# Optimization experiments

Hardware: AMD Instinct MI355X
Metric: run time of the kernel (lower is better)

Reference implementation:

```python
import jax, jax.numpy as jnp
import numpy as np

B, N, D, H = 4, 2048, 256, 4
DH = D // H          # 64
SCALE = DH ** (-0.5)
LN_EPS = 1e-5


def setup_inputs() -> dict:
    key = jax.random.key(0)
    ks = jax.random.split(key, 16)
    g = lambda k, shape, fan_in: jax.random.normal(k, shape, jnp.float32) / np.sqrt(fan_in)
    # Weights stored as [in, out] (pre-transposed vs torch Linear)
    return {
        "x0": jax.random.normal(ks[0], (B, N, D), jnp.float32),
        "x1": jax.random.normal(ks[1], (B, N, D), jnp.float32),
        "Wqk": g(ks[2], (D, D), D), "bqk": jnp.zeros((D,), jnp.float32),
        "Wv": g(ks[3], (D, D), D), "bv": jnp.zeros((D,), jnp.float32),
        "Wout": g(ks[4], (D, D), D), "bout": jnp.zeros((D,), jnp.float32),
        "Wf1": g(ks[5], (2 * D, 2 * D), 2 * D), "bf1": jnp.zeros((2 * D,), jnp.float32),
        "ln_g": jnp.ones((2 * D,), jnp.float32), "ln_b": jnp.zeros((2 * D,), jnp.float32),
        "Wf2": g(ks[6], (2 * D, D), 2 * D), "bf2": jnp.zeros((D,), jnp.float32),
    }


def _split_heads(t):
    # [B,N,D] -> [B,H,N,DH]
    b, n, _ = t.shape
    return t.reshape(b, n, H, DH).transpose(0, 2, 1, 3)


def _merge_heads(t):
    # [B,H,N,DH] -> [B,N,D]
    b, h, n, dh = t.shape
    return t.transpose(0, 2, 1, 3).reshape(b, n, h * dh)


def _layernorm(x, g, b):
    mu = jnp.mean(x, axis=-1, keepdims=True)
    var = jnp.mean(jnp.square(x - mu), axis=-1, keepdims=True)
    return (x - mu) * jax.lax.rsqrt(var + LN_EPS) * g + b


def reference(x0, x1, Wqk, bqk, Wv, bv, Wout, bout, Wf1, bf1, ln_g, ln_b, Wf2, bf2):
    qk0 = _split_heads(x0 @ Wqk + bqk)   # [B,H,N,DH]
    qk1 = _split_heads(x1 @ Wqk + bqk)
    v0 = _split_heads(x0 @ Wv + bv)
    v1 = _split_heads(x1 @ Wv + bv)

    ss = SCALE ** 0.5
    sim = jnp.einsum('bhid,bhjd->bhij', qk0 * ss, qk1 * ss)  # shared score matrix
    attn01 = jax.nn.softmax(sim, axis=-1)   # normalize over j
    attn10 = jax.nn.softmax(sim, axis=-2)   # normalize over i (== softmax(sim^T) transposed)
    m0 = jnp.einsum('bhij,bhjd->bhid', attn01, v1)
    m1 = jnp.einsum('bhji,bhjd->bhid', attn10, v0)

    m0 = _merge_heads(m0) @ Wout + bout   # [B,N,D]
    m1 = _merge_heads(m1) @ Wout + bout

    def ffn(x):
        h = x @ Wf1 + bf1                 # [B,N,2D]
        h = jax.nn.gelu(_layernorm(h, ln_g, ln_b), approximate=False)
        return h @ Wf2 + bf2              # [B,N,D]

    y0 = x0 + ffn(jnp.concatenate([x0, m0], axis=-1))
    y1 = x1 + ffn(jnp.concatenate([x1, m1], axis=-1))
    return (y0, y1)
```

## Files before the change

kernel.cpp:

```cpp
#include <hip/hip_runtime.h>
#include <hip/hip_bf16.h>
#include <math.h>

typedef __bf16 bf16;
typedef __attribute__((ext_vector_type(8))) __bf16 bf16x8;
typedef __attribute__((ext_vector_type(4))) __bf16 bf16x4;
typedef __attribute__((ext_vector_type(2))) __bf16 bf16x2;
typedef __attribute__((ext_vector_type(4))) float f32x4;
typedef __attribute__((ext_vector_type(16))) float f32x16;
typedef __attribute__((ext_vector_type(4))) unsigned u32x4;

#define MFMA(a,b,c)   __builtin_amdgcn_mfma_f32_16x16x32_bf16(a,b,c,0,0,0)
#define MFMA32(a,b,c) __builtin_amdgcn_mfma_f32_32x32x16_bf16(a,b,c,0,0,0)

static constexpr int Bb = 4, Nn = 2048, Hh = 4;
static constexpr float SS2 = 0.4246609001440095f;

__device__ __forceinline__ void lds16(const bf16* src, bf16* dst) {
  __builtin_amdgcn_global_load_lds(
      (const __attribute__((address_space(1))) void*)src,
      (__attribute__((address_space(3))) void*)dst, 16, 0, 0);
}

__device__ __forceinline__ f32x16 zero16() {
  f32x16 t;
#pragma unroll
  for (int i = 0; i < 16; ++i) t[i] = 0.f;
  return t;
}

__global__ __launch_bounds__(256) void prep_k(
    const float* Wqk, const float* Wv, const float* Wout, const float* bout,
    const float* Wf1, const float* Wf2, const float* x0, const float* x1,
    bf16* wqkv_t, bf16* wout_b, bf16* wfold_t, bf16* wf1b_t, bf16* wf2_t,
    bf16* xb0, bf16* xb1) {
  int id = blockIdx.x * 256 + threadIdx.x;
  if (id < 65536) { int k = id >> 8, n = id & 255; wqkv_t[n*256 + k] = (bf16)Wqk[id]; return; }
  id -= 65536;
  if (id < 65536) { int k = id >> 8, n = id & 255; wqkv_t[(256 + n)*256 + k] = (bf16)Wv[id]; return; }
  id -= 65536;
  if (id < 98304) {
    if (id < 65536) { wout_b[id] = (bf16)Wout[id]; }
    else { int id3 = id - 65536; int r = id3 >> 8, k = id3 & 255;
           wout_b[(256 + r)*256 + k] = (r == 0) ? (bf16)bout[k] : (bf16)0.f; }
    return; }
  id -= 98304;
  if (id < 131072) { int o = id & 511, k = id >> 9; wfold_t[o*512 + k] = (bf16)Wf1[k*512 + o]; return; }
  id -= 131072;
  if (id < 131072) { int o = id & 511, k = id >> 9; wf1b_t[o*256 + k] = (bf16)Wf1[(256 + k)*512 + o]; return; }
  id -= 131072;
  if (id < 131072) { int k = id >> 8, n = id & 255; wf2_t[n*512 + k] = (bf16)Wf2[id]; return; }
  id -= 131072;
  if (id < 1048576) {
    const float* xs = (id < 524288) ? x0 : x1;
    bf16* xd = (id < 524288) ? xb0 : xb1;
    int j = (id < 524288) ? id : id - 524288;
    f32x4 v = *reinterpret_cast<const f32x4*>(&xs[(size_t)j * 4]);
    bf16x4 o; o[0] = (bf16)v[0]; o[1] = (bf16)v[1]; o[2] = (bf16)v[2]; o[3] = (bf16)v[3];
    *reinterpret_cast<bf16x4*>(&xd[(size_t)j * 4]) = o;
  }
}

__global__ __launch_bounds__(256, 2) void qkvfold_k(
    const bf16* xb0, const bf16* xb1, const bf16* wqkv_t,
    const float* bqk, const float* bv,
    bf16* qks0, bf16* qks1, bf16* vT0, bf16* vT1,
    const bf16* wout_b, const bf16* wf1b_t, const float* bf1,
    bf16* wfold_t, float* bfold) {
  const int fid = blockIdx.x;
  const bool fold = fid >= 512;
  int bx, by, bz;
  if (!fold) {
    bx = ((fid & 7) << 3) + ((fid >> 3) & 7);
    by = (fid >> 6) & 3;
    bz = fid >> 8;
  } else {
    int id = fid - 512;
    bx = id % 3; by = id / 3; bz = 0;
  }

  const bf16* Aa = fold ? wout_b : (bz ? xb1 : xb0);
  const bf16* Wt = fold ? wf1b_t : wqkv_t;

  const int tid = threadIdx.x;
  const int lane = tid & 63;
  const int w = tid >> 6;
  const int wr = w >> 1, wc = w & 1;
  const int m0r = bx * 128;
  const int n0 = by * 128;
  const int r15 = lane & 15, g = lane >> 4, rb = r15 & 7;
  const int l3 = lane >> 3, l7 = lane & 7;
  const int swzc = (l7 ^ l3) * 8;

  __shared__ bf16 At[2][8192];
  __shared__ bf16 Bt[2][8192];

  const bf16* aA = Aa + (size_t)(m0r + w*32 + l3) * 256 + swzc;
  const bf16* bB = Wt + (size_t)(n0 + w*32 + l3) * 256 + swzc;
  const int adst = (w*32) * 64;

  auto stage = [&](int buf, int kc) {
#pragma unroll
    for (int i = 0; i < 4; i++)
      lds16(aA + kc*64 + (size_t)i * 8 * 256, &At[buf][adst + i*512]);
#pragma unroll
    for (int i = 0; i < 4; i++)
      lds16(bB + kc*64 + (size_t)i * 8 * 256, &Bt[buf][adst + i*512]);
  };

  f32x4 acc[4][4];
#pragma unroll
  for (int i = 0; i < 4; i++)
#pragma unroll
    for (int j = 0; j < 4; j++) acc[i][j] = f32x4{0.f, 0.f, 0.f, 0.f};

  const int rx0 = ((0*4 + g) ^ rb) << 4;
  const int rx1 = ((1*4 + g) ^ rb) << 4;

  auto compute = [&](int cur) {
    const char* Ap = (const char*)&At[cur][0];
    const char* Bp = (const char*)&Bt[cur][0];
    __builtin_amdgcn_s_setprio(1);
#pragma unroll
    for (int ks = 0; ks < 2; ++ks) {
      const int rx = ks ? rx1 : rx0;
      bf16x8 af[4], bfr[4];
#pragma unroll
      for (int mf = 0; mf < 4; ++mf)
        af[mf] = *reinterpret_cast<const bf16x8*>(Ap + (wr*64 + mf*16 + r15) * 128 + rx);
#pragma unroll
      for (int nf = 0; nf < 4; ++nf)
        bfr[nf] = *reinterpret_cast<const bf16x8*>(Bp + (wc*64 + nf*16 + r15) * 128 + rx);
#pragma unroll
      for (int mf = 0; mf < 4; ++mf)
#pragma unroll
        for (int nf = 0; nf < 4; ++nf)
          acc[mf][nf] = MFMA(af[mf], bfr[nf], acc[mf][nf]);
    }
    __builtin_amdgcn_s_setprio(0);
  };

  stage(0, 0);
  int cur = 0;
  for (int kc = 0; kc < 3; ++kc) {
    stage(cur ^ 1, kc + 1);
    asm volatile("s_waitcnt vmcnt(8)" ::: "memory");
    __builtin_amdgcn_sched_barrier(0);
    __builtin_amdgcn_s_barrier();
    __builtin_amdgcn_sched_barrier(0);
    compute(cur);
    asm volatile("s_waitcnt lgkmcnt(0)" ::: "memory");
    __builtin_amdgcn_sched_barrier(0);
    __builtin_amdgcn_s_barrier();
    __builtin_amdgcn_sched_barrier(0);
    cur ^= 1;
  }
  asm volatile("s_waitcnt vmcnt(0)" ::: "memory");
  __builtin_amdgcn_sched_barrier(0);
  __builtin_amdgcn_s_barrier();
  __builtin_amdgcn_sched_barrier(0);
  compute(cur);

  if (!fold) {
    bf16* qks = bz ? qks1 : qks0;
    bf16* vT  = bz ? vT1  : vT0;
#pragma unroll
    for (int mf = 0; mf < 4; ++mf)
#pragma unroll
      for (int nf = 0; nf < 4; ++nf) {
        f32x4 c = acc[mf][nf];
        int cg = n0 + wc*64 + nf*16 + r15;
#pragma unroll
        for (int r = 0; r < 4; ++r) {
          int rg = m0r + wr*64 + mf*16 + g*4 + r;
          int b = rg >> 11, n = rg & 2047;
          if (cg < 256) {
            float val = (c[r] + bqk[cg]) * SS2;
            int h = cg >> 6, dh = cg & 63;
            qks[(((size_t)(b*Hh + h)) * Nn + n) * 64 + dh] = (bf16)val;
          } else {
            int c2 = cg - 256;
            float val = c[r] + bv[c2];
            int h = c2 >> 6, dh = c2 & 63;
            vT[(((size_t)(b*Hh + h)) * 64 + dh) * Nn + n] = (bf16)val;
          }
        }
      }
  } else {
#pragma unroll
    for (int mf = 0; mf < 4; ++mf)
#pragma unroll
      for (int nf = 0; nf < 4; ++nf) {
        f32x4 c = acc[mf][nf];
        int cg = n0 + wc*64 + nf*16 + r15;
#pragma unroll
        for (int r = 0; r < 4; ++r) {
          int rg = m0r + wr*64 + mf*16 + g*4 + r;
          if (rg < 256) wfold_t[(size_t)cg * 512 + 256 + rg] = (bf16)c[r];
          else if (rg == 256) bfold[cg] = c[r] + bf1[cg];
        }
      }
  }
}

template<int MODE, int BN, int MINW, int REMAP>
__global__ __launch_bounds__(256, MINW) void gemm_k(
    const bf16* Aa0, const bf16* Aa1, const bf16* Ac0, const bf16* Ac1,
    const bf16* Wt, const float* bias,
    bf16* ob0, bf16* ob1, float* of0, float* of1) {
  constexpr int KD  = 512;
  constexpr int LDA = (MODE == 4) ? 512 : 256;
  constexpr int NKC = KD / 64;
  constexpr int NF  = BN / 32;

  int bx = blockIdx.x, by = blockIdx.y, bz = blockIdx.z;
  if constexpr (REMAP == 1) {
    int id = blockIdx.x + 64 * (blockIdx.y + 4 * blockIdx.z);
    bx = ((id & 7) << 3) + ((id >> 3) & 7);
    by = (id >> 6) & 3;
    bz = id >> 8;
  }

  const bf16* Aa = bz ? Aa1 : Aa0;
  const bf16* Ac = bz ? Ac1 : Ac0;
  bf16*  ob = bz ? ob1 : ob0;
  float* of = bz ? of1 : of0;

  const int tid = threadIdx.x;
  const int lane = tid & 63;
  const int w = tid >> 6;
  const int wr = w >> 1, wc = w & 1;
  const int m0r = bx * 128;
  const int n0 = by * BN;
  const int r15 = lane & 15, g = lane >> 4, rb = r15 & 7;
  const int l3 = lane >> 3, l7 = lane & 7;
  const int swzc = (l7 ^ l3) * 8;

  __shared__ bf16 At[2][8192];
  __shared__ bf16 Bt[2][BN * 64];

  const bf16* aA = Aa + (size_t)(m0r + w*32 + l3) * LDA + swzc;
  const bf16* aC = (MODE == 3) ? (Ac + (size_t)(m0r + w*32 + l3) * 256 + swzc) : nullptr;
  const bf16* bB = Wt + (size_t)(n0 + w*(BN/4) + l3) * KD + swzc;
  const int adst = (w*32) * 64;
  const int bdst = (w*(BN/4)) * 64;

  auto stage = [&](int buf, int kc) {
    const bf16* ab; int kcol;
    if constexpr (MODE == 3) {
      if (kc < 4) { ab = aA; kcol = kc * 64; } else { ab = aC; kcol = (kc - 4) * 64; }
    } else { ab = aA; kcol = kc * 64; }
#pragma unroll
    for (int i = 0; i < 4; i++)
      lds16(ab + kcol + (size_t)i * 8 * LDA, &At[buf][adst + i*512]);
#pragma unroll
    for (int i = 0; i < NF; i++)
      lds16(bB + kc*64 + (size_t)i * 8 * KD, &Bt[buf][bdst + i*512]);
  };

  f32x4 acc[4][NF];
#pragma unroll
  for (int i = 0; i < 4; i++)
#pragma unroll
    for (int j = 0; j < NF; j++) acc[i][j] = f32x4{0.f, 0.f, 0.f, 0.f};

  const int rx0 = ((0*4 + g) ^ rb) << 4;
  const int rx1 = ((1*4 + g) ^ rb) << 4;

  auto compute = [&](int cur) {
    const char* Ap = (const char*)&At[cur][0];
    const char* Bp = (const char*)&Bt[cur][0];
    __builtin_amdgcn_s_setprio(1);
#pragma unroll
    for (int ks = 0; ks < 2; ++ks) {
      const int rx = ks ? rx1 : rx0;
      bf16x8 af[4], bfr[NF];
#pragma unroll
      for (int mf = 0; mf < 4; ++mf)
        af[mf] = *reinterpret_cast<const bf16x8*>(Ap + (wr*64 + mf*16 + r15) * 128 + rx);
#pragma unroll
      for (int nf = 0; nf < NF; ++nf)
        bfr[nf] = *reinterpret_cast<const bf16x8*>(Bp + (wc*(BN/2) + nf*16 + r15) * 128 + rx);
#pragma unroll
      for (int mf = 0; mf < 4; ++mf)
#pragma unroll
        for (int nf = 0; nf < NF; ++nf)
          acc[mf][nf] = MFMA(af[mf], bfr[nf], acc[mf][nf]);
    }
    __builtin_amdgcn_s_setprio(0);
  };

  stage(0, 0);
  int cur = 0;
  for (int kc = 0; kc < NKC - 1; ++kc) {
    stage(cur ^ 1, kc + 1);
    if constexpr (NF == 4) asm volatile("s_waitcnt vmcnt(8)" ::: "memory");
    else                   asm volatile("s_waitcnt vmcnt(6)" ::: "memory");
    __builtin_amdgcn_sched_barrier(0);
    __builtin_amdgcn_s_barrier();
    __builtin_amdgcn_sched_barrier(0);
    compute(cur);
    asm volatile("s_waitcnt lgkmcnt(0)" ::: "memory");
    __builtin_amdgcn_sched_barrier(0);
    __builtin_amdgcn_s_barrier();
    __builtin_amdgcn_sched_barrier(0);
    cur ^= 1;
  }
  asm volatile("s_waitcnt vmcnt(0)" ::: "memory");
  __builtin_amdgcn_sched_barrier(0);
  __builtin_amdgcn_s_barrier();
  __builtin_amdgcn_sched_barrier(0);
  compute(cur);

#pragma unroll
  for (int mf = 0; mf < 4; ++mf)
#pragma unroll
    for (int nf = 0; nf < NF; ++nf) {
      f32x4 c = acc[mf][nf];
      int cg = n0 + wc*(BN/2) + nf*16 + r15;
#pragma unroll
      for (int r = 0; r < 4; ++r) {
        int rg = m0r + wr*64 + mf*16 + g*4 + r;
        if constexpr (MODE == 3) {
          ob[(size_t)rg * 512 + cg] = (bf16)(c[r] + bias[cg]);
        } else {
          of[(size_t)rg * 256 + cg] = c[r] + bias[cg] + (float)Ac[(size_t)rg * 256 + cg];
        }
      }
    }
}

__global__ __launch_bounds__(512, 4) void attn_k(
    const bf16* qks0, const bf16* qks1, const bf16* vT0, const bf16* vT1,
    bf16* m0o, bf16* m1o) {
  const int B = blockIdx.x + 16 * (blockIdx.y + 16 * blockIdx.z);
  const int xcd = B & 7, kk = B >> 3;
  const int group = 4 * xcd + (kk >> 4);
  const int it = kk & 15;
  const int bh = group & 15, dir = group >> 4;

  const bf16* Q  = (dir ? qks1 : qks0) + (size_t)bh * (Nn * 64);
  const bf16* Kp = (dir ? qks0 : qks1) + (size_t)bh * (Nn * 64);
  const bf16* Vp = (dir ? vT0  : vT1 ) + (size_t)bh * (64 * Nn);
  bf16* out = dir ? m1o : m0o;
  const int b = bh >> 2, h = bh & 3;

  const int tid = threadIdx.x, lane = tid & 63, w = tid >> 6;
  const int ig = w >> 1, hj = w & 1;
  const int l31 = lane & 31, hi = lane >> 5, xr = l31 & 7;
  const int iw = it * 128 + ig * 32;

  __shared__ char smem[65536];
  bf16* KV = (bf16*)smem;
  const int kbase = hj * 8192;
  const int vbase = 16384 + hj * 8192;

  bf16x8 qf[4];
#pragma unroll
  for (int kt = 0; kt < 4; ++kt)
    qf[kt] = *reinterpret_cast<const bf16x8*>(
        &Q[(size_t)(iw + l31) * 64 + kt*16 + hi*8]);

  f32x16 acc[2]; acc[0] = zero16(); acc[1] = zero16();
  float rsum = 0.f;

  const int l3 = lane >> 3, l7 = lane & 7;
  const int swz = ((l7 ^ l3) * 8);
  const bf16* ks0 = Kp + (size_t)(ig*16 +     l3) * 64 + swz;
  const bf16* ks1 = Kp + (size_t)(ig*16 + 8 + l3) * 64 + swz;
  const bf16* vs0 = Vp + (size_t)(ig*16 +     l3) * 2048 + swz;
  const bf16* vs1 = Vp + (size_t)(ig*16 + 8 + l3) * 2048 + swz;
  const int kd0 = (ig*16    ) * 64;
  const int kd1 = (ig*16 + 8) * 64;

  auto stage = [&](int buf, int j0) {
    lds16(ks0 + (size_t)j0 * 64, KV + kbase + buf*4096 + kd0);
    lds16(ks1 + (size_t)j0 * 64, KV + kbase + buf*4096 + kd1);
    lds16(vs0 + j0,              KV + vbase + buf*4096 + kd0);
    lds16(vs1 + j0,              KV + vbase + buf*4096 + kd1);
  };

  int kby[2][4], vby[2][4];
#pragma unroll
  for (int jm = 0; jm < 2; ++jm)
#pragma unroll
    for (int kt = 0; kt < 4; ++kt)
      kby[jm][kt] = (jm*32 + l31) * 128 + (((2*kt + hi) ^ xr) << 4);
#pragma unroll
  for (int nt = 0; nt < 2; ++nt)
#pragma unroll
    for (int gg = 0; gg < 4; ++gg)
      vby[nt][gg] = (nt*32 + l31) * 128 + (((2*gg + hi) ^ xr) << 4);

  auto compute_tile = [&](int cur) {
    const char* Kb = (const char*)(KV + kbase + cur*4096);
    const char* Vb = (const char*)(KV + vbase + cur*4096);
    f32x16 st[2];
    __builtin_amdgcn_s_setprio(1);
#pragma unroll
    for (int jm = 0; jm < 2; ++jm) {
      f32x16 t = zero16();
#pragma unroll
      for (int kt = 0; kt < 4; ++kt) {
        bf16x8 kf = *reinterpret_cast<const bf16x8*>(Kb + kby[jm][kt]);
        t = MFMA32(kf, qf[kt], t);
      }
      st[jm] = t;
    }
    __builtin_amdgcn_s_setprio(0);
    bf16x8 pa[4];
#pragma unroll
    for (int jm = 0; jm < 2; ++jm) {
      unsigned dw[8];
#pragma unroll
      for (int s = 0; s < 8; ++s) {
        float e0 = __builtin_amdgcn_exp2f(st[jm][2*s]);
        float e1 = __builtin_amdgcn_exp2f(st[jm][2*s + 1]);
        rsum += e0 + e1;
        asm("v_cvt_pk_bf16_f32 %0, %1, %2" : "=v"(dw[s]) : "v"(e0), "v"(e1));
      }
#pragma unroll
      for (int kt2 = 0; kt2 < 2; ++kt2) {
        unsigned a0 = dw[4*kt2 + 0], b0 = dw[4*kt2 + 2];
        unsigned a1 = dw[4*kt2 + 1], b1 = dw[4*kt2 + 3];
        asm volatile("v_permlane32_swap_b32 %0, %1" : "+v"(a0), "+v"(b0));
        asm volatile("v_permlane32_swap_b32 %0, %1" : "+v"(a1), "+v"(b1));
        u32x4 uu; uu[0] = a0; uu[1] = a1; uu[2] = b0; uu[3] = b1;
        pa[jm*2 + kt2] = __builtin_bit_cast(bf16x8, uu);
      }
    }
    __builtin_amdgcn_s_setprio(1);
#pragma unroll
    for (int gg = 0; gg < 4; ++gg) {
#pragma unroll
      for (int nt = 0; nt < 2; ++nt) {
        bf16x8 vf = *reinterpret_cast<const bf16x8*>(Vb + vby[nt][gg]);
        acc[nt] = MFMA32(pa[gg], vf, acc[nt]);
      }
    }
    __builtin_amdgcn_s_setprio(0);
  };

  const int jt0 = hj << 4;
  stage(0, jt0 << 6);
  int cur = 0;
  for (int t = 0; t < 15; ++t) {
    stage(cur ^ 1, (jt0 + t + 1) << 6);
    asm volatile("s_waitcnt vmcnt(4)" ::: "memory");
    __builtin_amdgcn_sched_barrier(0);
    __builtin_amdgcn_s_barrier();
    __builtin_amdgcn_sched_barrier(0);
    compute_tile(cur);
    asm volatile("s_waitcnt lgkmcnt(0)" ::: "memory");
    __builtin_amdgcn_sched_barrier(0);
    __builtin_amdgcn_s_barrier();
    __builtin_amdgcn_sched_barrier(0);
    cur ^= 1;
  }
  asm volatile("s_waitcnt vmcnt(0)" ::: "memory");
  __builtin_amdgcn_sched_barrier(0);
  __builtin_amdgcn_s_barrier();
  __builtin_amdgcn_sched_barrier(0);
  compute_tile(cur);

  rsum += __shfl_xor(rsum, 32);
  __syncthreads();
  float* Ex = (float*)smem;
  if (hj == 1) {
#pragma unroll
    for (int nt = 0; nt < 2; ++nt)
#pragma unroll
      for (int r = 0; r < 16; ++r)
        Ex[(ig*33 + nt*16 + r) * 64 + lane] = acc[nt][r];
    Ex[(ig*33 + 32) * 64 + lane] = rsum;
  }
  __syncthreads();
  if (hj == 0) {
    float tot = rsum + Ex[(ig*33 + 32) * 64 + lane];
    float* Rt2 = (float*)(smem + 49152);
    if (lane < 32) Rt2[ig*32 + l31] = tot;
    f32x4 rv[4];
#pragma unroll
    for (int q = 0; q < 4; ++q)
      rv[q] = *reinterpret_cast<const f32x4*>(&Rt2[ig*32 + 8*q + 4*hi]);
#pragma unroll
    for (int r = 0; r < 16; ++r) {
      float inv = 1.0f / rv[r >> 2][r & 3];
      int row = iw + (r & 3) + 8*(r >> 2) + 4*hi;
#pragma unroll
      for (int nt = 0; nt < 2; ++nt) {
        float o = acc[nt][r] + Ex[(ig*33 + nt*16 + r) * 64 + lane];
        int col = h*64 + nt*32 + l31;
        out[((size_t)b * Nn + row) * 256 + col] = (bf16)(o * inv);
      }
    }
  }
}

__global__ __launch_bounds__(256) void ln_gelu_k(
    bf16* hg, const float* g, const float* bb) {
  const int row = (blockIdx.x << 2) + (threadIdx.x >> 6);
  const int lane = threadIdx.x & 63;
  bf16* hr = hg + (size_t)row * 512 + lane * 8;
  bf16x8 v = *reinterpret_cast<const bf16x8*>(hr);
  float f[8];
  float s = 0.f, sq = 0.f;
#pragma unroll
  for (int i = 0; i < 8; ++i) { f[i] = (float)v[i]; s += f[i]; sq += f[i]*f[i]; }
#pragma unroll
  for (int m = 1; m < 64; m <<= 1) { s += __shfl_xor(s, m); sq += __shfl_xor(sq, m); }
  float mu = s * (1.f / 512.f);
  float var = sq * (1.f / 512.f) - mu * mu;
  float rsv = rsqrtf(var + 1e-5f);
  f32x4 g0 = *reinterpret_cast<const f32x4*>(&g[lane*8]);
  f32x4 g1 = *reinterpret_cast<const f32x4*>(&g[lane*8 + 4]);
  f32x4 b0 = *reinterpret_cast<const f32x4*>(&bb[lane*8]);
  f32x4 b1 = *reinterpret_cast<const f32x4*>(&bb[lane*8 + 4]);
  bf16x8 o;
#pragma unroll
  for (int i = 0; i < 8; ++i) {
    float gv = (i < 4) ? g0[i] : g1[i-4];
    float bv = (i < 4) ? b0[i] : b1[i-4];
    float xn = (f[i] - mu) * rsv * gv + bv;
    float ge = 0.5f * xn * (1.f + erff(xn * 0.70710678118f));
    o[i] = (bf16)ge;
  }
  *reinterpret_cast<bf16x8*>(hr) = o;
}

extern "C" void kernel_launch(void* const* d_in, const int* in_sizes, int n_in,
                              void* d_out, int out_size, void* d_ws, size_t ws_size,
                              hipStream_t stream) {
  (void)in_sizes; (void)n_in; (void)out_size; (void)ws_size;
  const float* x0   = (const float*)d_in[0];
  const float* x1   = (const float*)d_in[1];
  const float* Wqk  = (const float*)d_in[2];
  const float* bqk  = (const float*)d_in[3];
  const float* Wv   = (const float*)d_in[4];
  const float* bv   = (const float*)d_in[5];
  const float* Wout = (const float*)d_in[6];
  const float* bout = (const float*)d_in[7];
  const float* Wf1  = (const float*)d_in[8];
  const float* bf1  = (const float*)d_in[9];
  const float* ln_g = (const float*)d_in[10];
  const float* ln_b = (const float*)d_in[11];
  const float* Wf2  = (const float*)d_in[12];
  const float* bf2  = (const float*)d_in[13];
  float* y = (float*)d_out;

  bf16* p = (bf16*)d_ws;
  bf16* wqkv_t = p; p += 131072;
  bf16* wout_b = p; p += 98304;
  bf16* wfold_t = p; p += 262144;
  bf16* wf1b_t = p; p += 131072;
  bf16* wf2_t  = p; p += 131072;
  float* bfold = (float*)p; p += 1024;
  bf16* xb0  = p; p += 2097152;
  bf16* xb1  = p; p += 2097152;
  bf16* qks0 = p; p += 2097152;
  bf16* qks1 = p; p += 2097152;
  bf16* vT0  = p; p += 2097152;
  bf16* vT1  = p; p += 2097152;
  bf16* m0   = p; p += 2097152;
  bf16* m1   = p; p += 2097152;
  bf16* hg0  = p; p += 4194304;
  bf16* hg1  = p; p += 4194304;

  dim3 blk(256);
  prep_k<<<6528, blk, 0, stream>>>(Wqk, Wv, Wout, bout, Wf1, Wf2, x0, x1,
                                   wqkv_t, wout_b, wfold_t, wf1b_t, wf2_t, xb0, xb1);
  qkvfold_k<<<dim3(524), blk, 0, stream>>>(
      xb0, xb1, wqkv_t, bqk, bv, qks0, qks1, vT0, vT1,
      wout_b, wf1b_t, bf1, wfold_t, bfold);
  attn_k<<<dim3(16, 16, 2), dim3(512), 0, stream>>>(qks0, qks1, vT0, vT1, m0, m1);
  gemm_k<3,128,2,1><<<dim3(64, 4, 2), blk, 0, stream>>>(
      xb0, xb1, m0, m1, wfold_t, bfold,
      hg0, hg1, nullptr, nullptr);
  ln_gelu_k<<<dim3(4096), blk, 0, stream>>>(hg0, ln_g, ln_b);
  gemm_k<4,64,3,0><<<dim3(64, 4, 2), blk, 0, stream>>>(
      hg0, hg1, xb0, xb1, wf2_t, bf2,
      nullptr, nullptr, y, y + 2097152);
}
```

Before: 120.6 us.

## Fuse LayerNorm and GELU into the first FFN GEMM epilogue

Adds a dedicated GEMM kernel in which each 512-thread block computes a 64-row tile across all 512 output columns. This lets the block reduce per-row mean and variance in-register and through LDS, then apply LayerNorm, affine and exact GELU before writing bf16. It removes the separate ln_gelu pass and the extra read and write of the hidden activations, and drops the MODE 3 branch from the generic GEMM. The second FFN GEMM also switches to the remapped block ordering. The cost is a large LDS footprint, about 144KB double-buffered, which allows only one block per CU. It also brings a cross-wave reduction with extra barriers in the epilogue and a full weight re-read per block.

Result: slower. 124.2 us (+3.0%).

```diff
diff --git a/kernel.cpp b/kernel.cpp
--- a/kernel.cpp
+++ b/kernel.cpp
@@ -203,6 +203,174 @@
   }
 }
 
+__global__ __launch_bounds__(512, 2) void gemm3f_k(
+    const bf16* Aa0, const bf16* Aa1, const bf16* Ac0, const bf16* Ac1,
+    const bf16* Wt, const float* bias,
+    const float* lng, const float* lnb,
+    bf16* ob0, bf16* ob1) {
+  const int id = blockIdx.x;
+  const int bz = id >> 7, bx = id & 127;
+  const bf16* Aa = bz ? Aa1 : Aa0;
+  const bf16* Ac = bz ? Ac1 : Ac0;
+  bf16* ob = bz ? ob1 : ob0;
+
+  const int tid = threadIdx.x;
+  const int lane = tid & 63;
+  const int w = tid >> 6;
+  const int m0r = bx * 64;
+  const int r15 = lane & 15, g = lane >> 4, rb = r15 & 7;
+  const int l3 = lane >> 3, l7 = lane & 7;
+  const int swzc = (l7 ^ l3) * 8;
+
+  __shared__ bf16 At[2][4096];
+  __shared__ bf16 Bt[2][32768];
+
+  const bf16* aA = Aa + (size_t)(m0r + w*8 + l3) * 256 + swzc;
+  const bf16* aC = Ac + (size_t)(m0r + w*8 + l3) * 256 + swzc;
+  const bf16* bB = Wt + (size_t)(w*64 + l3) * 512 + swzc;
+  const int adst = (w*8) * 64;
+  const int bdst = (w*64) * 64;
+
+  auto stage = [&](int buf, int kc) {
+    const bf16* ab = (kc < 4) ? aA : aC;
+    const int kcol = (kc < 4) ? kc*64 : (kc - 4)*64;
+    lds16(ab + kcol, &At[buf][adst]);
+#pragma unroll
+    for (int i = 0; i < 8; i++)
+      lds16(bB + kc*64 + (size_t)i * 8 * 512, &Bt[buf][bdst + i*512]);
+  };
+
+  f32x4 acc[4][4];
+#pragma unroll
+  for (int i = 0; i < 4; i++)
+#pragma unroll
+    for (int j = 0; j < 4; j++) acc[i][j] = f32x4{0.f, 0.f, 0.f, 0.f};
+
+  const int rx0 = ((0*4 + g) ^ rb) << 4;
+  const int rx1 = ((1*4 + g) ^ rb) << 4;
+
+  auto compute = [&](int cur) {
+    const char* Ap = (const char*)&At[cur][0];
+    const char* Bp = (const char*)&Bt[cur][0];
+    __builtin_amdgcn_s_setprio(1);
+#pragma unroll
+    for (int ks = 0; ks < 2; ++ks) {
+      const int rx = ks ? rx1 : rx0;
+      bf16x8 af[4], bfr[4];
+#pragma unroll
+      for (int mf = 0; mf < 4; ++mf)
+        af[mf] = *reinterpret_cast<const bf16x8*>(Ap + (mf*16 + r15) * 128 + rx);
+#pragma unroll
+      for (int nf = 0; nf < 4; ++nf)
+        bfr[nf] = *reinterpret_cast<const bf16x8*>(Bp + (w*64 + nf*16 + r15) * 128 + rx);
+#pragma unroll
+      for (int mf = 0; mf < 4; ++mf)
+#pragma unroll
+        for (int nf = 0; nf < 4; ++nf)
+          acc[mf][nf] = MFMA(af[mf], bfr[nf], acc[mf][nf]);
+    }
+    __builtin_amdgcn_s_setprio(0);
+  };
+
+  stage(0, 0);
+  int cur = 0;
+  for (int kc = 0; kc < 7; ++kc) {
+    stage(cur ^ 1, kc + 1);
+    asm volatile("s_waitcnt vmcnt(9)" ::: "memory");
+    __builtin_amdgcn_sched_barrier(0);
+    __builtin_amdgcn_s_barrier();
+    __builtin_amdgcn_sched_barrier(0);
+    compute(cur);
+    asm volatile("s_waitcnt lgkmcnt(0)" ::: "memory");
+    __builtin_amdgcn_sched_barrier(0);
+    __builtin_amdgcn_s_barrier();
+    __builtin_amdgcn_sched_barrier(0);
+    cur ^= 1;
+  }
+  asm volatile("s_waitcnt vmcnt(0)" ::: "memory");
+  __builtin_amdgcn_sched_barrier(0);
+  __builtin_amdgcn_s_barrier();
+  __builtin_amdgcn_sched_barrier(0);
+  compute(cur);
+
+  float bch[4];
+#pragma unroll
+  for (int nf = 0; nf < 4; ++nf) bch[nf] = bias[w*64 + nf*16 + r15];
+
+  float s_[4][4], s2_[4][4];
+#pragma unroll
+  for (int mf = 0; mf < 4; ++mf)
+#pragma unroll
+    for (int r = 0; r < 4; ++r) {
+      float s = 0.f, s2 = 0.f;
+#pragma unroll
+      for (int nf = 0; nf < 4; ++nf) {
+        float v = acc[mf][nf][r] + bch[nf];
+        s += v; s2 += v * v;
+      }
+      s_[mf][r] = s; s2_[mf][r] = s2;
+    }
+#pragma unroll
+  for (int mf = 0; mf < 4; ++mf)
+#pragma unroll
+    for (int r = 0; r < 4; ++r) {
+#pragma unroll
+      for (int m = 1; m < 16; m <<= 1) {
+        s_[mf][r]  += __shfl_xor(s_[mf][r],  m);
+        s2_[mf][r] += __shfl_xor(s2_[mf][r], m);
+      }
+    }
+  __syncthreads();
+  float* sred  = (float*)&At[0][0];
+  float* rstat = sred + 1024;
+  if (r15 == 0) {
+#pragma unroll
+    for (int mf = 0; mf < 4; ++mf)
+#pragma unroll
+      for (int r = 0; r < 4; ++r) {
+        int row = mf*16 + g*4 + r;
+        sred[(w*64 + row)*2    ] = s_[mf][r];
+        sred[(w*64 + row)*2 + 1] = s2_[mf][r];
+      }
+  }
+  __syncthreads();
+  if (tid < 64) {
+    float S = 0.f, S2 = 0.f;
+#pragma unroll
+    for (int wv = 0; wv < 8; ++wv) {
+      S  += sred[(wv*64 + tid)*2];
+      S2 += sred[(wv*64 + tid)*2 + 1];
+    }
+    float mu = S * (1.f/512.f);
+    float var = S2 * (1.f/512.f) - mu*mu;
+    rstat[tid*2]     = mu;
+    rstat[tid*2 + 1] = rsqrtf(var + 1e-5f);
+  }
+  __syncthreads();
+  float gch[4], bth[4];
+#pragma unroll
+  for (int nf = 0; nf < 4; ++nf) {
+    int col = w*64 + nf*16 + r15;
+    gch[nf] = lng[col]; bth[nf] = lnb[col];
+  }
+#pragma unroll
+  for (int mf = 0; mf < 4; ++mf)
+#pragma unroll
+    for (int r = 0; r < 4; ++r) {
+      int rowl = mf*16 + g*4 + r;
+      float mu  = rstat[rowl*2];
+      float rsv = rstat[rowl*2 + 1];
+#pragma unroll
+      for (int nf = 0; nf < 4; ++nf) {
+        int col = w*64 + nf*16 + r15;
+        float val = acc[mf][nf][r] + bch[nf];
+        float xn = (val - mu) * rsv * gch[nf] + bth[nf];
+        float ge = 0.5f * xn * (1.f + erff(xn * 0.70710678118f));
+        ob[(size_t)(m0r + rowl) * 512 + col] = (bf16)ge;
+      }
+    }
+}
+
 template<int MODE, int BN, int MINW, int REMAP>
 __global__ __launch_bounds__(256, MINW) void gemm_k(
     const bf16* Aa0, const bf16* Aa1, const bf16* Ac0, const bf16* Ac1,
@@ -225,6 +393,7 @@
   const bf16* Ac = bz ? Ac1 : Ac0;
   bf16*  ob = bz ? ob1 : ob0;
   float* of = bz ? of1 : of0;
+  (void)ob;
 
   const int tid = threadIdx.x;
   const int lane = tid & 63;
@@ -240,19 +409,14 @@
   __shared__ bf16 Bt[2][BN * 64];
 
   const bf16* aA = Aa + (size_t)(m0r + w*32 + l3) * LDA + swzc;
-  const bf16* aC = (MODE == 3) ? (Ac + (size_t)(m0r + w*32 + l3) * 256 + swzc) : nullptr;
   const bf16* bB = Wt + (size_t)(n0 + w*(BN/4) + l3) * KD + swzc;
   const int adst = (w*32) * 64;
   const int bdst = (w*(BN/4)) * 64;
 
   auto stage = [&](int buf, int kc) {
-    const bf16* ab; int kcol;
-    if constexpr (MODE == 3) {
-      if (kc < 4) { ab = aA; kcol = kc * 64; } else { ab = aC; kcol = (kc - 4) * 64; }
-    } else { ab = aA; kcol = kc * 64; }
 #pragma unroll
     for (int i = 0; i < 4; i++)
-      lds16(ab + kcol + (size_t)i * 8 * LDA, &At[buf][adst + i*512]);
+      lds16(aA + kc*64 + (size_t)i * 8 * LDA, &At[buf][adst + i*512]);
 #pragma unroll
     for (int i = 0; i < NF; i++)
       lds16(bB + kc*64 + (size_t)i * 8 * KD, &Bt[buf][bdst + i*512]);
@@ -321,11 +485,7 @@
 #pragma unroll
       for (int r = 0; r < 4; ++r) {
         int rg = m0r + wr*64 + mf*16 + g*4 + r;
-        if constexpr (MODE == 3) {
-          ob[(size_t)rg * 512 + cg] = (bf16)(c[r] + bias[cg]);
-        } else {
-          of[(size_t)rg * 256 + cg] = c[r] + bias[cg] + (float)Ac[(size_t)rg * 256 + cg];
-        }
+        of[(size_t)rg * 256 + cg] = c[r] + bias[cg] + (float)Ac[(size_t)rg * 256 + cg];
       }
     }
 }
@@ -495,37 +655,6 @@
       }
     }
   }
-}
-
-__global__ __launch_bounds__(256) void ln_gelu_k(
-    bf16* hg, const float* g, const float* bb) {
-  const int row = (blockIdx.x << 2) + (threadIdx.x >> 6);
-  const int lane = threadIdx.x & 63;
-  bf16* hr = hg + (size_t)row * 512 + lane * 8;
-  bf16x8 v = *reinterpret_cast<const bf16x8*>(hr);
-  float f[8];
-  float s = 0.f, sq = 0.f;
-#pragma unroll
-  for (int i = 0; i < 8; ++i) { f[i] = (float)v[i]; s += f[i]; sq += f[i]*f[i]; }
-#pragma unroll
-  for (int m = 1; m < 64; m <<= 1) { s += __shfl_xor(s, m); sq += __shfl_xor(sq, m); }
-  float mu = s * (1.f / 512.f);
-  float var = sq * (1.f / 512.f) - mu * mu;
-  float rsv = rsqrtf(var + 1e-5f);
-  f32x4 g0 = *reinterpret_cast<const f32x4*>(&g[lane*8]);
-  f32x4 g1 = *reinterpret_cast<const f32x4*>(&g[lane*8 + 4]);
-  f32x4 b0 = *reinterpret_cast<const f32x4*>(&bb[lane*8]);
-  f32x4 b1 = *reinterpret_cast<const f32x4*>(&bb[lane*8 + 4]);
-  bf16x8 o;
-#pragma unroll
-  for (int i = 0; i < 8; ++i) {
-    float gv = (i < 4) ? g0[i] : g1[i-4];
-    float bv = (i < 4) ? b0[i] : b1[i-4];
-    float xn = (f[i] - mu) * rsv * gv + bv;
-    float ge = 0.5f * xn * (1.f + erff(xn * 0.70710678118f));
-    o[i] = (bf16)ge;
-  }
-  *reinterpret_cast<bf16x8*>(hr) = o;
 }
 
 extern "C" void kernel_launch(void* const* d_in, const int* in_sizes, int n_in,
@@ -573,11 +702,9 @@
       xb0, xb1, wqkv_t, bqk, bv, qks0, qks1, vT0, vT1,
       wout_b, wf1b_t, bf1, wfold_t, bfold);
   attn_k<<<dim3(16, 16, 2), dim3(512), 0, stream>>>(qks0, qks1, vT0, vT1, m0, m1);
-  gemm_k<3,128,2,1><<<dim3(64, 4, 2), blk, 0, stream>>>(
-      xb0, xb1, m0, m1, wfold_t, bfold,
-      hg0, hg1, nullptr, nullptr);
-  ln_gelu_k<<<dim3(4096), blk, 0, stream>>>(hg0, ln_g, ln_b);
-  gemm_k<4,64,3,0><<<dim3(64, 4, 2), blk, 0, stream>>>(
+  gemm3f_k<<<dim3(256), dim3(512), 0, stream>>>(
+      xb0, xb1, m0, m1, wfold_t, bfold, ln_g, ln_b, hg0, hg1);
+  gemm_k<4,64,3,1><<<dim3(64, 4, 2), blk, 0, stream>>>(
       hg0, hg1, xb0, xb1, wf2_t, bf2,
       nullptr, nullptr, y, y + 2097152);
 }
```

## Stage V-transpose epilogue through swizzled LDS for coalesced stores; drop sched barriers

Applied to the files above, without the earlier changes.

The projection epilogue for the V half now writes bias-added bf16 tiles into a swizzled LDS buffer. It then reads them back so each thread emits 16-byte contiguous stores along the sequence dimension of vT, replacing scattered 2-byte transposed global writes. It also removes sched_barrier fences around the s_barriers in the attention main loop, letting the compiler interleave instructions across them. The LDS staging adds two block syncs and reuses the A-tile buffer. Removing the fences risks reordering memory operations relative to the hand-placed waitcnts.

New measurement: 112.9 us. -6.4%, faster.

```diff
diff --git a/kernel.cpp b/kernel.cpp
--- a/kernel.cpp
+++ b/kernel.cpp
@@ -164,28 +164,52 @@
   if (!fold) {
     bf16* qks = bz ? qks1 : qks0;
     bf16* vT  = bz ? vT1  : vT0;
-#pragma unroll
-    for (int mf = 0; mf < 4; ++mf)
-#pragma unroll
-      for (int nf = 0; nf < 4; ++nf) {
-        f32x4 c = acc[mf][nf];
-        int cg = n0 + wc*64 + nf*16 + r15;
-#pragma unroll
-        for (int r = 0; r < 4; ++r) {
-          int rg = m0r + wr*64 + mf*16 + g*4 + r;
-          int b = rg >> 11, n = rg & 2047;
-          if (cg < 256) {
+    if (by < 2) {
+#pragma unroll
+      for (int mf = 0; mf < 4; ++mf)
+#pragma unroll
+        for (int nf = 0; nf < 4; ++nf) {
+          f32x4 c = acc[mf][nf];
+          int cg = n0 + wc*64 + nf*16 + r15;
+#pragma unroll
+          for (int r = 0; r < 4; ++r) {
+            int rg = m0r + wr*64 + mf*16 + g*4 + r;
+            int b = rg >> 11, n = rg & 2047;
             float val = (c[r] + bqk[cg]) * SS2;
             int h = cg >> 6, dh = cg & 63;
             qks[(((size_t)(b*Hh + h)) * Nn + n) * 64 + dh] = (bf16)val;
-          } else {
-            int c2 = cg - 256;
-            float val = c[r] + bv[c2];
-            int h = c2 >> 6, dh = c2 & 63;
-            vT[(((size_t)(b*Hh + h)) * 64 + dh) * Nn + n] = (bf16)val;
           }
         }
-      }
+    } else {
+      __syncthreads();
+      char* T = (char*)&At[0][0];
+#pragma unroll
+      for (int mf = 0; mf < 4; ++mf)
+#pragma unroll
+        for (int nf = 0; nf < 4; ++nf) {
+          f32x4 c = acc[mf][nf];
+          int cl = wc*64 + nf*16 + r15;
+          float bvv = bv[(by - 2) * 128 + cl];
+          int rl = wr*64 + mf*16 + g*4;
+          bf16x4 o;
+          o[0] = (bf16)(c[0] + bvv); o[1] = (bf16)(c[1] + bvv);
+          o[2] = (bf16)(c[2] + bvv); o[3] = (bf16)(c[3] + bvv);
+          int boff = cl*256 + ((rl*2) ^ ((cl & 15) << 4));
+          *reinterpret_cast<bf16x4*>(T + boff) = o;
+        }
+      __syncthreads();
+      const int cl = tid >> 1, nh = tid & 1;
+      const int c2 = (by - 2) * 128 + cl;
+      const int h = c2 >> 6, dh = c2 & 63;
+      const int b = m0r >> 11, nbase = (m0r & 2047) + nh*64;
+      bf16* dst = vT + (((size_t)(b*Hh + h)) * 64 + dh) * 2048 + nbase;
+#pragma unroll
+      for (int i = 0; i < 8; ++i) {
+        int nl = nh*64 + i*8;
+        int boff = cl*256 + ((nl*2) ^ ((cl & 15) << 4));
+        *reinterpret_cast<uint4*>(dst + i*8) = *reinterpret_cast<const uint4*>(T + boff);
+      }
+    }
   } else {
 #pragma unroll
     for (int mf = 0; mf < 4; ++mf)
@@ -447,20 +471,14 @@
   for (int t = 0; t < 15; ++t) {
     stage(cur ^ 1, (jt0 + t + 1) << 6);
     asm volatile("s_waitcnt vmcnt(4)" ::: "memory");
-    __builtin_amdgcn_sched_barrier(0);
     __builtin_amdgcn_s_barrier();
-    __builtin_amdgcn_sched_barrier(0);
     compute_tile(cur);
     asm volatile("s_waitcnt lgkmcnt(0)" ::: "memory");
-    __builtin_amdgcn_sched_barrier(0);
     __builtin_amdgcn_s_barrier();
-    __builtin_amdgcn_sched_barrier(0);
     cur ^= 1;
   }
   asm volatile("s_waitcnt vmcnt(0)" ::: "memory");
-  __builtin_amdgcn_sched_barrier(0);
   __builtin_amdgcn_s_barrier();
-  __builtin_amdgcn_sched_barrier(0);
   compute_tile(cur);
 
   rsum += __shfl_xor(rsum, 32);
```
